# Kernel tuning notes

Hardware: AMD Instinct MI355X
Metric: run time of the kernel (lower is better)

Reference implementation:

```python
import jax, jax.numpy as jnp
import numpy as np

B, CIN, COUT, H, W = 16, 96, 96, 96, 96
K = 3   # hidden_kernels (conv), odd -> same padding
A = 3   # attn_kernels, odd -> stride-1 unfold preserves H*W positions


def _conv(x, w, p):
    # NCHW conv with symmetric padding p, stride 1, no bias
    return jax.lax.conv_general_dilated(
        x, w, window_strides=(1, 1), padding=[(p, p), (p, p)],
        dimension_numbers=("NCHW", "OIHW", "NCHW"))


def _unfold_nonoverlap(y, a):
    # torch nn.Unfold(a, stride=a): [B,C,H,W] -> [B, C*a*a, L], channel-major (c,kh,kw)
    b, c, h, w = y.shape
    hb, wb = h // a, w // a
    y = y.reshape(b, c, hb, a, wb, a).transpose(0, 1, 3, 5, 2, 4)
    return y.reshape(b, c * a * a, hb * wb)


def _unfold_stride1(y, a):
    # torch nn.Unfold(a, padding=a//2): [B,C,H,W] -> [B, C*a*a, H*W]
    b, c, h, w = y.shape
    p = a // 2
    yp = jnp.pad(y, ((0, 0), (0, 0), (p, p), (p, p)))
    # small fixed a*a loop (9 shifts), channel-major (c,kh,kw) ordering
    patches = jnp.stack([yp[:, :, i:i + h, j:j + w]
                         for i in range(a) for j in range(a)], axis=2)
    return patches.reshape(b, c * a * a, h * w)


def setup_inputs() -> dict:
    key = jax.random.key(0)
    kx, k1, k2, k3 = jax.random.split(key, 4)
    x = jax.random.normal(kx, (B, CIN, H, W), dtype=jnp.float32)
    W1 = jax.random.normal(k1, (COUT, CIN, K, K), dtype=jnp.float32) * 0.05
    W2 = jax.random.normal(k2, (COUT, CIN, K, K), dtype=jnp.float32) * 0.05
    W3 = jax.random.normal(k3, (COUT, CIN, K, K), dtype=jnp.float32) * 0.05
    return {"x": x, "W1": W1, "W2": W2, "W3": W3}


def reference(x, W1, W2, W3):
    a, c, p = A, COUT, K // 2
    b = x.shape[0]
    y1 = _unfold_nonoverlap(_conv(x, W1, p), a)   # [B, C*a^2, L]
    y2 = _unfold_nonoverlap(_conv(x, W2, p), a)   # [B, C*a^2, L]
    L = y1.shape[-1]
    y1 = y1.reshape(b, c, a * a, L).transpose(0, 2, 1, 3)  # [B, a^2, C, L]
    y2 = y2.reshape(b, c, a * a, L).transpose(0, 2, 3, 1)  # [B, a^2, L, C]
    attn = jnp.einsum("bkcl,bkld->bkcd", y1, y2)           # [B, a^2, C, C]
    # torch: transpose(1,3).flatten(2) -> [B, C, C*a^2], then scale + softmax(dim=2)
    attn = attn.transpose(0, 3, 2, 1).reshape(b, c, c * a * a)
    attn = jax.nn.softmax(attn / np.float32(np.sqrt(c * a * a)), axis=2)
    v = _unfold_stride1(_conv(x, W3, p), a)        # [B, C*a^2, H*W]
    out = jnp.einsum("bcm,bml->bcl", attn, v)      # [B, C, H*W]
    return out.reshape(b, c, H, W)
```

## Files before the change

### kernel.cpp

```cpp
#include <hip/hip_runtime.h>
#include <math.h>
#include <stdint.h>

constexpr int BB  = 16;
constexpr int CH  = 96;
constexpr int HH  = 96;
constexpr int WW  = 96;
constexpr int HWI = HH * WW;
constexpr int CHW = CH * HWI;
constexpr int IMG = BB * CHW;
constexpr int ATT = BB * CH * CH * 9;
constexpr int WPK = 27 * 6 * 64 * 8;

typedef short short8 __attribute__((ext_vector_type(8)));
typedef float floatx4 __attribute__((ext_vector_type(4)));

__device__ __forceinline__ ushort f2bf(float f) {
  union { float f; unsigned u; } v; v.f = f;
  unsigned r = (v.u + 0x7fffu + ((v.u >> 16) & 1u)) >> 16;
  return (ushort)r;
}
__device__ __forceinline__ float bf2f(ushort h) {
  union { float f; unsigned u; } v; v.u = ((unsigned)h) << 16;
  return v.f;
}

__device__ __forceinline__ void gl_lds_b128(const void* g, void* s) {
  auto gp = (const __attribute__((address_space(1))) void*)(uintptr_t)g;
  auto sp = (__attribute__((address_space(3))) void*)(uintptr_t)s;
  __builtin_amdgcn_global_load_lds(gp, sp, 16, 0, 0);
}

__global__ __launch_bounds__(256) void prepack(
    const float* __restrict__ src, ushort* __restrict__ dst)
{
  const int g = blockIdx.y;
  const int p = blockIdx.x * 256 + threadIdx.x;
  const float* s = src + (size_t)g * WPK;
  ushort* d = dst + (size_t)g * WPK;
  const int j    = p & 7;
  const int lane = (p >> 3) & 63;
  const int rest = p >> 9;
  const int mt = rest % 6;
  const int kc = rest / 6;
  const int m  = mt * 16 + (lane & 15);
  const int k  = kc * 32 + (lane >> 4) * 8 + j;
  const int ci = k % 96;
  const int o  = k / 96;
  d[p] = f2bf(s[m * 864 + ci * 9 + o]);
}

__global__ __launch_bounds__(256, 2) void conv_mfma(
    const float* __restrict__ X, const ushort* __restrict__ Wpk,
    float* __restrict__ Y, int wbstride)
{
  const int b    = blockIdx.y;
  const int tile = blockIdx.x;
  const int ty0  = (tile / 6) * 12;
  const int tx0  = (tile % 6) * 16;
  const int tid  = threadIdx.x;
  const int lane = tid & 63;
  const int w    = tid >> 6;
  const int nc   = lane & 15;
  const int q    = lane >> 4;

  __shared__ __attribute__((aligned(16))) ushort Xs[252 * 104];
  __shared__ __attribute__((aligned(16))) ushort Wl[2][3072];

  const ushort* wp = Wpk + (size_t)b * wbstride;

  {
    gl_lds_b128(wp + w * 512 + lane * 8,
                (ushort*)Wl[0] + __builtin_amdgcn_readfirstlane(w * 512));
    if (w < 2)
      gl_lds_b128(wp + (w + 4) * 512 + lane * 8,
                  (ushort*)Wl[0] + __builtin_amdgcn_readfirstlane((w + 4) * 512));
  }

  if (tid < 252) {
    const int ly = tid / 18, lx = tid % 18;
    const int gy = ty0 - 1 + ly, gx = tx0 - 1 + lx;
    const bool inb = ((unsigned)gy < 96u) & ((unsigned)gx < 96u);
    const float* src = X + (size_t)b * CHW + gy * WW + gx;
    ushort* dst = &Xs[tid * 104];
#pragma unroll 4
    for (int cg = 0; cg < 24; ++cg) {
      float f0 = 0.f, f1 = 0.f, f2 = 0.f, f3 = 0.f;
      if (inb) {
        const float* s = src + (size_t)(cg * 4) * HWI;
        f0 = s[0]; f1 = s[HWI]; f2 = s[2 * HWI]; f3 = s[3 * HWI];
      }
      ushort4 u;
      u.x = f2bf(f0); u.y = f2bf(f1); u.z = f2bf(f2); u.w = f2bf(f3);
      *(ushort4*)(dst + cg * 4) = u;
    }
  }
  __syncthreads();

  floatx4 acc[6][3];
#pragma unroll
  for (int mt = 0; mt < 6; ++mt)
#pragma unroll
    for (int t = 0; t < 3; ++t)
#pragma unroll
      for (int r = 0; r < 4; ++r) acc[mt][t][r] = 0.f;

  for (int ch = 0; ch < 27; ++ch) {
    if (ch < 26) {
      const ushort* src = wp + (size_t)(ch + 1) * 3072;
      ushort* dstb = (ushort*)Wl[(ch + 1) & 1];
      gl_lds_b128(src + w * 512 + lane * 8,
                  dstb + __builtin_amdgcn_readfirstlane(w * 512));
      if (w < 2)
        gl_lds_b128(src + (w + 4) * 512 + lane * 8,
                    dstb + __builtin_amdgcn_readfirstlane((w + 4) * 512));
    }

    const ushort* wb = Wl[ch & 1];
    const int o  = ch / 3;
    const int cc = ch - o * 3;
    const int dy = o / 3, dx = o - dy * 3;
    const int pc = nc + dx;
    const int cib = cc * 32 + q * 8;

    short8 bfr[3];
#pragma unroll
    for (int t = 0; t < 3; ++t) {
      const int pix = (3 * w + t + dy) * 18 + pc;
      bfr[t] = *(const short8*)(&Xs[pix * 104 + cib]);
    }

#pragma unroll
    for (int mt = 0; mt < 6; ++mt) {
      const short8 af = *(const short8*)(wb + mt * 512 + lane * 8);
#pragma unroll
      for (int t = 0; t < 3; ++t)
        acc[mt][t] = __builtin_amdgcn_mfma_f32_16x16x32_bf16(
            af, bfr[t], acc[mt][t], 0, 0, 0);
    }
    __syncthreads();
  }

  float* yb = Y + (size_t)b * CHW;
#pragma unroll
  for (int mt = 0; mt < 6; ++mt)
#pragma unroll
    for (int t = 0; t < 3; ++t) {
      const int yy = ty0 + 3 * w + t;
      const int xx = tx0 + nc;
#pragma unroll
      for (int r = 0; r < 4; ++r) {
        const int co = mt * 16 + q * 4 + r;
        yb[(size_t)co * HWI + yy * WW + xx] = acc[mt][t][r];
      }
    }
}

__global__ __launch_bounds__(256, 2) void conv_dual_mfma(
    const float* __restrict__ X,
    const ushort* __restrict__ WpkA, const ushort* __restrict__ WpkB,
    float* __restrict__ YA, float* __restrict__ YB)
{
  const int b    = blockIdx.y;
  const int tile = blockIdx.x;
  const int ty0  = (tile / 6) * 12;
  const int tx0  = (tile % 6) * 16;
  const int tid  = threadIdx.x;
  const int lane = tid & 63;
  const int w    = tid >> 6;
  const int nc   = lane & 15;
  const int q    = lane >> 4;

  __shared__ __attribute__((aligned(16))) ushort Xs[252 * 104];
  __shared__ __attribute__((aligned(16))) ushort Wl[2][6144];

  {
#pragma unroll
    for (int i = 0; i < 3; ++i) {
      const int p  = w + 4 * i;
      const int cv = p / 6;
      const int pt = p - cv * 6;
      const ushort* src = (cv ? WpkB : WpkA) + pt * 512 + lane * 8;
      gl_lds_b128(src, (ushort*)Wl[0] +
                  __builtin_amdgcn_readfirstlane(cv * 3072 + pt * 512));
    }
  }

  if (tid < 252) {
    const int ly = tid / 18, lx = tid % 18;
    const int gy = ty0 - 1 + ly, gx = tx0 - 1 + lx;
    const bool inb = ((unsigned)gy < 96u) & ((unsigned)gx < 96u);
    const float* src = X + (size_t)b * CHW + gy * WW + gx;
    ushort* dst = &Xs[tid * 104];
#pragma unroll 4
    for (int cg = 0; cg < 24; ++cg) {
      float f0 = 0.f, f1 = 0.f, f2 = 0.f, f3 = 0.f;
      if (inb) {
        const float* s = src + (size_t)(cg * 4) * HWI;
        f0 = s[0]; f1 = s[HWI]; f2 = s[2 * HWI]; f3 = s[3 * HWI];
      }
      ushort4 u;
      u.x = f2bf(f0); u.y = f2bf(f1); u.z = f2bf(f2); u.w = f2bf(f3);
      *(ushort4*)(dst + cg * 4) = u;
    }
  }
  __syncthreads();

  floatx4 accA[6][3], accB[6][3];
#pragma unroll
  for (int mt = 0; mt < 6; ++mt)
#pragma unroll
    for (int t = 0; t < 3; ++t)
#pragma unroll
      for (int r = 0; r < 4; ++r) { accA[mt][t][r] = 0.f; accB[mt][t][r] = 0.f; }

  for (int ch = 0; ch < 27; ++ch) {
    if (ch < 26) {
      const size_t coff = (size_t)(ch + 1) * 3072;
      ushort* dstb = (ushort*)Wl[(ch + 1) & 1];
#pragma unroll
      for (int i = 0; i < 3; ++i) {
        const int p  = w + 4 * i;
        const int cv = p / 6;
        const int pt = p - cv * 6;
        const ushort* src = (cv ? WpkB : WpkA) + coff + pt * 512 + lane * 8;
        gl_lds_b128(src, dstb +
                    __builtin_amdgcn_readfirstlane(cv * 3072 + pt * 512));
      }
    }

    const ushort* wb = Wl[ch & 1];
    const int o  = ch / 3;
    const int cc = ch - o * 3;
    const int dy = o / 3, dx = o - dy * 3;
    const int pc = nc + dx;
    const int cib = cc * 32 + q * 8;

    short8 bfr[3];
#pragma unroll
    for (int t = 0; t < 3; ++t) {
      const int pix = (3 * w + t + dy) * 18 + pc;
      bfr[t] = *(const short8*)(&Xs[pix * 104 + cib]);
    }

#pragma unroll
    for (int mt = 0; mt < 6; ++mt) {
      const short8 afA = *(const short8*)(wb + mt * 512 + lane * 8);
#pragma unroll
      for (int t = 0; t < 3; ++t)
        accA[mt][t] = __builtin_amdgcn_mfma_f32_16x16x32_bf16(
            afA, bfr[t], accA[mt][t], 0, 0, 0);
      const short8 afB = *(const short8*)(wb + 3072 + mt * 512 + lane * 8);
#pragma unroll
      for (int t = 0; t < 3; ++t)
        accB[mt][t] = __builtin_amdgcn_mfma_f32_16x16x32_bf16(
            afB, bfr[t], accB[mt][t], 0, 0, 0);
    }
    __syncthreads();
  }

  float* yA = YA + (size_t)b * CHW;
  float* yB = YB + (size_t)b * CHW;
#pragma unroll
  for (int mt = 0; mt < 6; ++mt)
#pragma unroll
    for (int t = 0; t < 3; ++t) {
      const int yy = ty0 + 3 * w + t;
      const int xx = tx0 + nc;
#pragma unroll
      for (int r = 0; r < 4; ++r) {
        const int co = mt * 16 + q * 4 + r;
        yA[(size_t)co * HWI + yy * WW + xx] = accA[mt][t][r];
        yB[(size_t)co * HWI + yy * WW + xx] = accB[mt][t][r];
      }
    }
}

__global__ __launch_bounds__(1024) void attn_mfma(
    const float* __restrict__ Y1, const float* __restrict__ Y2,
    float* __restrict__ attnT)
{
  const int b  = blockIdx.x / 9;
  const int k  = blockIdx.x % 9;
  const int kh = k / 3, kw = k % 3;
  const int tid  = threadIdx.x;
  const int lane = tid & 63;
  const int wv   = tid >> 6;

  __shared__ ushort Ah[96 * 72], Al[96 * 72], Bh[96 * 72], Bl[96 * 72];

  const float* y1b = Y1 + (size_t)b * CHW;
  const float* y2b = Y2 + (size_t)b * CHW;

  const int mg = wv / 3;
  const int ng = wv % 3;
  const int cn = lane & 15;
  const int q  = lane >> 4;

  floatx4 acc[2][2];
#pragma unroll
  for (int i = 0; i < 2; ++i)
#pragma unroll
    for (int j = 0; j < 2; ++j)
#pragma unroll
      for (int r = 0; r < 4; ++r) acc[i][j][r] = 0.f;

  const int sj = tid & 31;
  const int sg = tid >> 5;
  const int scol = 3 * sj + kw;

  for (int s = 0; s < 16; ++s) {
    __syncthreads();
#pragma unroll
    for (int c8 = 0; c8 < 3; ++c8) {
      const int c = c8 * 32 + sg;
      const int cbase = c * 72;
#pragma unroll
      for (int ii = 0; ii < 2; ++ii) {
        const int row = 3 * (s * 2 + ii) + kh;
        const int p   = ii * 32 + sj;
        const size_t goff = (size_t)c * HWI + row * WW + scol;
        const float v1 = y1b[goff];
        const float v2 = y2b[goff];
        const ushort h1 = f2bf(v1);
        const ushort h2 = f2bf(v2);
        Ah[cbase + p] = h1;
        Al[cbase + p] = f2bf(v1 - bf2f(h1));
        Bh[cbase + p] = h2;
        Bl[cbase + p] = f2bf(v2 - bf2f(h2));
      }
    }
    __syncthreads();

    if (wv < 9) {
#pragma unroll
      for (int kc = 0; kc < 2; ++kc) {
        short8 ah[2], al[2], bh[2], bl[2];
#pragma unroll
        for (int t = 0; t < 2; ++t) {
          const int offA = ((mg * 2 + t) * 16 + cn) * 72 + kc * 32 + q * 8;
          ah[t] = *(const short8*)(&Ah[offA]);
          al[t] = *(const short8*)(&Al[offA]);
          const int offB = ((ng * 2 + t) * 16 + cn) * 72 + kc * 32 + q * 8;
          bh[t] = *(const short8*)(&Bh[offB]);
          bl[t] = *(const short8*)(&Bl[offB]);
        }
#pragma unroll
        for (int i = 0; i < 2; ++i)
#pragma unroll
          for (int j = 0; j < 2; ++j) {
            acc[i][j] = __builtin_amdgcn_mfma_f32_16x16x32_bf16(
                ah[i], bh[j], acc[i][j], 0, 0, 0);
            acc[i][j] = __builtin_amdgcn_mfma_f32_16x16x32_bf16(
                ah[i], bl[j], acc[i][j], 0, 0, 0);
            acc[i][j] = __builtin_amdgcn_mfma_f32_16x16x32_bf16(
                al[i], bh[j], acc[i][j], 0, 0, 0);
          }
      }
    }
  }

  if (wv < 9) {
#pragma unroll
    for (int i = 0; i < 2; ++i)
#pragma unroll
      for (int j = 0; j < 2; ++j)
#pragma unroll
        for (int r = 0; r < 4; ++r) {
          const int c = (mg * 2 + i) * 16 + q * 4 + r;
          const int d = (ng * 2 + j) * 16 + cn;
          attnT[((size_t)(b * CH + d) * CH + c) * 9 + k] = acc[i][j][r];
        }
  }
}

__global__ __launch_bounds__(256) void softmax_k(
    const float* __restrict__ attnT, float* __restrict__ attnW)
{
  const int bd = blockIdx.x;
  const float* src = attnT + (size_t)bd * 864;
  float* dst = attnW + (size_t)bd * 864;
  const float rs = 0.0340216824f;
  const int tid = threadIdx.x;

  float v0 = src[tid];
  float v1 = src[tid + 256];
  float v2 = src[tid + 512];
  float v3 = (tid < 96) ? src[tid + 768] : -3.0e38f;

  float mx = fmaxf(fmaxf(v0, v1), fmaxf(v2, v3));

  __shared__ float red[256];
  red[tid] = mx;
  __syncthreads();
#pragma unroll
  for (int s = 128; s > 0; s >>= 1) {
    if (tid < s) red[tid] = fmaxf(red[tid], red[tid + s]);
    __syncthreads();
  }
  mx = red[0];
  __syncthreads();

  const float e0 = expf((v0 - mx) * rs);
  const float e1 = expf((v1 - mx) * rs);
  const float e2 = expf((v2 - mx) * rs);
  const float e3 = (tid < 96) ? expf((v3 - mx) * rs) : 0.f;

  red[tid] = e0 + e1 + e2 + e3;
  __syncthreads();
#pragma unroll
  for (int s = 128; s > 0; s >>= 1) {
    if (tid < s) red[tid] += red[tid + s];
    __syncthreads();
  }
  const float inv = 1.f / red[0];

  dst[tid]       = e0 * inv;
  dst[tid + 256] = e1 * inv;
  dst[tid + 512] = e2 * inv;
  if (tid < 96) dst[tid + 768] = e3 * inv;
}

extern "C" void kernel_launch(void* const* d_in, const int* in_sizes, int n_in,
                              void* d_out, int out_size, void* d_ws, size_t ws_size,
                              hipStream_t stream)
{
  const float* x  = (const float*)d_in[0];
  const float* W1 = (const float*)d_in[1];
  const float* W2 = (const float*)d_in[2];
  const float* W3 = (const float*)d_in[3];

  float* ws    = (float*)d_ws;
  float* Y1    = ws;
  float* Y2    = ws + (size_t)IMG;
  float* attnT = ws + 2 * (size_t)IMG;
  float* attnW = attnT + ATT;
  ushort* pk   = (ushort*)(ws + 2 * (size_t)IMG + 2 * (size_t)ATT);
  ushort* pkW1 = pk;
  ushort* pkW2 = pk + WPK;
  ushort* pkW3 = pk + 2 * (size_t)WPK;
  ushort* pkAW = pk + 3 * (size_t)WPK;
  float* Y3    = Y1;

  const dim3 cgrid(48, BB);

  prepack  <<<dim3(324, 1),  256, 0, stream>>>(W1, pkW1);
  prepack  <<<dim3(324, 1),  256, 0, stream>>>(W2, pkW2);
  prepack  <<<dim3(324, 1),  256, 0, stream>>>(W3, pkW3);

  conv_dual_mfma<<<cgrid, 256, 0, stream>>>(x, pkW1, pkW2, Y1, Y2);

  attn_mfma<<<BB * 9, 1024, 0, stream>>>(Y1, Y2, attnT);
  softmax_k<<<BB * CH, 256, 0, stream>>>(attnT, attnW);

  prepack  <<<dim3(324, BB), 256, 0, stream>>>(attnW, pkAW);

  conv_mfma<<<cgrid, 256, 0, stream>>>(x, pkW3, Y3, 0);
  conv_mfma<<<cgrid, 256, 0, stream>>>(Y3, pkAW, (float*)d_out, WPK);
}
```

Measured before the change: 370.6 us.

## Split attention reduction over spatial chunks, pre-split hi/lo bf16, store Y3 as bf16

The attention Gram kernel now splits the spatial reduction into four chunks, launching four times as many smaller 256-thread blocks. Each block writes a partial result, and the softmax kernel sums the four partials before normalizing. The dual conv now writes hi/lo bf16 pairs packed in a uint, so the attention kernel no longer does that conversion. The intermediate V conv output is stored as bf16 through a templated conv kernel, which halves its memory traffic. Partial buffers reuse the output and workspace as scratch, which adds extra partial-sum reads and relies on careful aliasing of attnW as both a partial buffer and the softmax output.

```diff
diff --git a/kernel.cpp b/kernel.cpp
--- a/kernel.cpp
+++ b/kernel.cpp
@@ -23,6 +23,11 @@
 __device__ __forceinline__ float bf2f(ushort h) {
   union { float f; unsigned u; } v; v.u = ((unsigned)h) << 16;
   return v.f;
+}
+__device__ __forceinline__ uint packhl(float v) {
+  const ushort h = f2bf(v);
+  const ushort l = f2bf(v - bf2f(h));
+  return (uint)h | ((uint)l << 16);
 }
 
 __device__ __forceinline__ void gl_lds_b128(const void* g, void* s) {
@@ -50,9 +55,10 @@
   d[p] = f2bf(s[m * 864 + ci * 9 + o]);
 }
 
-__global__ __launch_bounds__(256, 2) void conv_mfma(
-    const float* __restrict__ X, const ushort* __restrict__ Wpk,
-    float* __restrict__ Y, int wbstride)
+template<bool INBF, bool OUTBF>
+__global__ __launch_bounds__(256, 2) void conv_mfma_t(
+    const void* __restrict__ Xv, const ushort* __restrict__ Wpk,
+    void* __restrict__ Yv, int wbstride)
 {
   const int b    = blockIdx.y;
   const int tile = blockIdx.x;
@@ -75,6 +81,132 @@
     if (w < 2)
       gl_lds_b128(wp + (w + 4) * 512 + lane * 8,
                   (ushort*)Wl[0] + __builtin_amdgcn_readfirstlane((w + 4) * 512));
+  }
+
+  if (tid < 252) {
+    const int ly = tid / 18, lx = tid % 18;
+    const int gy = ty0 - 1 + ly, gx = tx0 - 1 + lx;
+    const bool inb = ((unsigned)gy < 96u) & ((unsigned)gx < 96u);
+    ushort* dst = &Xs[tid * 104];
+    if constexpr (INBF) {
+      const ushort* src = (const ushort*)Xv + (size_t)b * CHW + gy * WW + gx;
+#pragma unroll 4
+      for (int cg = 0; cg < 24; ++cg) {
+        ushort u0 = 0, u1 = 0, u2 = 0, u3 = 0;
+        if (inb) {
+          const ushort* s = src + (size_t)(cg * 4) * HWI;
+          u0 = s[0]; u1 = s[HWI]; u2 = s[2 * HWI]; u3 = s[3 * HWI];
+        }
+        ushort4 u; u.x = u0; u.y = u1; u.z = u2; u.w = u3;
+        *(ushort4*)(dst + cg * 4) = u;
+      }
+    } else {
+      const float* src = (const float*)Xv + (size_t)b * CHW + gy * WW + gx;
+#pragma unroll 4
+      for (int cg = 0; cg < 24; ++cg) {
+        float f0 = 0.f, f1 = 0.f, f2 = 0.f, f3 = 0.f;
+        if (inb) {
+          const float* s = src + (size_t)(cg * 4) * HWI;
+          f0 = s[0]; f1 = s[HWI]; f2 = s[2 * HWI]; f3 = s[3 * HWI];
+        }
+        ushort4 u;
+        u.x = f2bf(f0); u.y = f2bf(f1); u.z = f2bf(f2); u.w = f2bf(f3);
+        *(ushort4*)(dst + cg * 4) = u;
+      }
+    }
+  }
+  __syncthreads();
+
+  floatx4 acc[6][3];
+#pragma unroll
+  for (int mt = 0; mt < 6; ++mt)
+#pragma unroll
+    for (int t = 0; t < 3; ++t)
+#pragma unroll
+      for (int r = 0; r < 4; ++r) acc[mt][t][r] = 0.f;
+
+  for (int ch = 0; ch < 27; ++ch) {
+    if (ch < 26) {
+      const ushort* src = wp + (size_t)(ch + 1) * 3072;
+      ushort* dstb = (ushort*)Wl[(ch + 1) & 1];
+      gl_lds_b128(src + w * 512 + lane * 8,
+                  dstb + __builtin_amdgcn_readfirstlane(w * 512));
+      if (w < 2)
+        gl_lds_b128(src + (w + 4) * 512 + lane * 8,
+                    dstb + __builtin_amdgcn_readfirstlane((w + 4) * 512));
+    }
+
+    const ushort* wb = Wl[ch & 1];
+    const int o  = ch / 3;
+    const int cc = ch - o * 3;
+    const int dy = o / 3, dx = o - dy * 3;
+    const int pc = nc + dx;
+    const int cib = cc * 32 + q * 8;
+
+    short8 bfr[3];
+#pragma unroll
+    for (int t = 0; t < 3; ++t) {
+      const int pix = (3 * w + t + dy) * 18 + pc;
+      bfr[t] = *(const short8*)(&Xs[pix * 104 + cib]);
+    }
+
+#pragma unroll
+    for (int mt = 0; mt < 6; ++mt) {
+      const short8 af = *(const short8*)(wb + mt * 512 + lane * 8);
+#pragma unroll
+      for (int t = 0; t < 3; ++t)
+        acc[mt][t] = __builtin_amdgcn_mfma_f32_16x16x32_bf16(
+            af, bfr[t], acc[mt][t], 0, 0, 0);
+    }
+    __syncthreads();
+  }
+
+#pragma unroll
+  for (int mt = 0; mt < 6; ++mt)
+#pragma unroll
+    for (int t = 0; t < 3; ++t) {
+      const int yy = ty0 + 3 * w + t;
+      const int xx = tx0 + nc;
+#pragma unroll
+      for (int r = 0; r < 4; ++r) {
+        const int co = mt * 16 + q * 4 + r;
+        const size_t off = (size_t)co * HWI + yy * WW + xx;
+        if constexpr (OUTBF)
+          ((ushort*)Yv + (size_t)b * CHW)[off] = f2bf(acc[mt][t][r]);
+        else
+          ((float*)Yv + (size_t)b * CHW)[off] = acc[mt][t][r];
+      }
+    }
+}
+
+__global__ __launch_bounds__(256, 2) void conv_dual_mfma(
+    const float* __restrict__ X,
+    const ushort* __restrict__ WpkA, const ushort* __restrict__ WpkB,
+    uint* __restrict__ YA, uint* __restrict__ YB)
+{
+  const int b    = blockIdx.y;
+  const int tile = blockIdx.x;
+  const int ty0  = (tile / 6) * 12;
+  const int tx0  = (tile % 6) * 16;
+  const int tid  = threadIdx.x;
+  const int lane = tid & 63;
+  const int w    = tid >> 6;
+  const int nc   = lane & 15;
+  const int q    = lane >> 4;
+
+  __shared__ __attribute__((aligned(16))) ushort Xs[252 * 104];
+  __shared__ __attribute__((aligned(16))) ushort Wl[2][6144];
+
+  {
+#pragma unroll
+    for (int i = 0; i < 3; ++i) {
+      const int p  = w + 4 * i;
+      const int cv = p / 6;
+      const int pt = p - cv * 6;
+      const ushort* src = (cv ? WpkB : WpkA) + pt * 512 + lane * 8;
+      gl_lds_b128(src, (ushort*)Wl[0] +
+                  __builtin_amdgcn_readfirstlane(cv * 3072 + pt * 512));
+    }
   }
 
   if (tid < 252) {
@@ -97,115 +229,6 @@
   }
   __syncthreads();
 
-  floatx4 acc[6][3];
-#pragma unroll
-  for (int mt = 0; mt < 6; ++mt)
-#pragma unroll
-    for (int t = 0; t < 3; ++t)
-#pragma unroll
-      for (int r = 0; r < 4; ++r) acc[mt][t][r] = 0.f;
-
-  for (int ch = 0; ch < 27; ++ch) {
-    if (ch < 26) {
-      const ushort* src = wp + (size_t)(ch + 1) * 3072;
-      ushort* dstb = (ushort*)Wl[(ch + 1) & 1];
-      gl_lds_b128(src + w * 512 + lane * 8,
-                  dstb + __builtin_amdgcn_readfirstlane(w * 512));
-      if (w < 2)
-        gl_lds_b128(src + (w + 4) * 512 + lane * 8,
-                    dstb + __builtin_amdgcn_readfirstlane((w + 4) * 512));
-    }
-
-    const ushort* wb = Wl[ch & 1];
-    const int o  = ch / 3;
-    const int cc = ch - o * 3;
-    const int dy = o / 3, dx = o - dy * 3;
-    const int pc = nc + dx;
-    const int cib = cc * 32 + q * 8;
-
-    short8 bfr[3];
-#pragma unroll
-    for (int t = 0; t < 3; ++t) {
-      const int pix = (3 * w + t + dy) * 18 + pc;
-      bfr[t] = *(const short8*)(&Xs[pix * 104 + cib]);
-    }
-
-#pragma unroll
-    for (int mt = 0; mt < 6; ++mt) {
-      const short8 af = *(const short8*)(wb + mt * 512 + lane * 8);
-#pragma unroll
-      for (int t = 0; t < 3; ++t)
-        acc[mt][t] = __builtin_amdgcn_mfma_f32_16x16x32_bf16(
-            af, bfr[t], acc[mt][t], 0, 0, 0);
-    }
-    __syncthreads();
-  }
-
-  float* yb = Y + (size_t)b * CHW;
-#pragma unroll
-  for (int mt = 0; mt < 6; ++mt)
-#pragma unroll
-    for (int t = 0; t < 3; ++t) {
-      const int yy = ty0 + 3 * w + t;
-      const int xx = tx0 + nc;
-#pragma unroll
-      for (int r = 0; r < 4; ++r) {
-        const int co = mt * 16 + q * 4 + r;
-        yb[(size_t)co * HWI + yy * WW + xx] = acc[mt][t][r];
-      }
-    }
-}
-
-__global__ __launch_bounds__(256, 2) void conv_dual_mfma(
-    const float* __restrict__ X,
-    const ushort* __restrict__ WpkA, const ushort* __restrict__ WpkB,
-    float* __restrict__ YA, float* __restrict__ YB)
-{
-  const int b    = blockIdx.y;
-  const int tile = blockIdx.x;
-  const int ty0  = (tile / 6) * 12;
-  const int tx0  = (tile % 6) * 16;
-  const int tid  = threadIdx.x;
-  const int lane = tid & 63;
-  const int w    = tid >> 6;
-  const int nc   = lane & 15;
-  const int q    = lane >> 4;
-
-  __shared__ __attribute__((aligned(16))) ushort Xs[252 * 104];
-  __shared__ __attribute__((aligned(16))) ushort Wl[2][6144];
-
-  {
-#pragma unroll
-    for (int i = 0; i < 3; ++i) {
-      const int p  = w + 4 * i;
-      const int cv = p / 6;
-      const int pt = p - cv * 6;
-      const ushort* src = (cv ? WpkB : WpkA) + pt * 512 + lane * 8;
-      gl_lds_b128(src, (ushort*)Wl[0] +
-                  __builtin_amdgcn_readfirstlane(cv * 3072 + pt * 512));
-    }
-  }
-
-  if (tid < 252) {
-    const int ly = tid / 18, lx = tid % 18;
-    const int gy = ty0 - 1 + ly, gx = tx0 - 1 + lx;
-    const bool inb = ((unsigned)gy < 96u) & ((unsigned)gx < 96u);
-    const float* src = X + (size_t)b * CHW + gy * WW + gx;
-    ushort* dst = &Xs[tid * 104];
-#pragma unroll 4
-    for (int cg = 0; cg < 24; ++cg) {
-      float f0 = 0.f, f1 = 0.f, f2 = 0.f, f3 = 0.f;
-      if (inb) {
-        const float* s = src + (size_t)(cg * 4) * HWI;
-        f0 = s[0]; f1 = s[HWI]; f2 = s[2 * HWI]; f3 = s[3 * HWI];
-      }
-      ushort4 u;
-      u.x = f2bf(f0); u.y = f2bf(f1); u.z = f2bf(f2); u.w = f2bf(f3);
-      *(ushort4*)(dst + cg * 4) = u;
-    }
-  }
-  __syncthreads();
-
   floatx4 accA[6][3], accB[6][3];
 #pragma unroll
   for (int mt = 0; mt < 6; ++mt)
@@ -259,8 +282,8 @@
     __syncthreads();
   }
 
-  float* yA = YA + (size_t)b * CHW;
-  float* yB = YB + (size_t)b * CHW;
+  uint* yA = YA + (size_t)b * CHW;
+  uint* yB = YB + (size_t)b * CHW;
 #pragma unroll
   for (int mt = 0; mt < 6; ++mt)
 #pragma unroll
@@ -270,18 +293,22 @@
 #pragma unroll
       for (int r = 0; r < 4; ++r) {
         const int co = mt * 16 + q * 4 + r;
-        yA[(size_t)co * HWI + yy * WW + xx] = accA[mt][t][r];
-        yB[(size_t)co * HWI + yy * WW + xx] = accB[mt][t][r];
-      }
-    }
-}
-
-__global__ __launch_bounds__(1024) void attn_mfma(
-    const float* __restrict__ Y1, const float* __restrict__ Y2,
-    float* __restrict__ attnT)
-{
-  const int b  = blockIdx.x / 9;
-  const int k  = blockIdx.x % 9;
+        yA[(size_t)co * HWI + yy * WW + xx] = packhl(accA[mt][t][r]);
+        yB[(size_t)co * HWI + yy * WW + xx] = packhl(accB[mt][t][r]);
+      }
+    }
+}
+
+__global__ __launch_bounds__(256) void attn_mfma(
+    const uint* __restrict__ Y1, const uint* __restrict__ Y2,
+    float* __restrict__ P0, float* __restrict__ P1,
+    float* __restrict__ P2, float* __restrict__ P3)
+{
+  const int bi = blockIdx.x;
+  const int b  = bi / 36;
+  const int r9 = bi % 36;
+  const int k  = r9 >> 2;
+  const int qd = r9 & 3;
   const int kh = k / 3, kw = k % 3;
   const int tid  = threadIdx.x;
   const int lane = tid & 63;
@@ -289,19 +316,19 @@
 
   __shared__ ushort Ah[96 * 72], Al[96 * 72], Bh[96 * 72], Bl[96 * 72];
 
-  const float* y1b = Y1 + (size_t)b * CHW;
-  const float* y2b = Y2 + (size_t)b * CHW;
-
-  const int mg = wv / 3;
-  const int ng = wv % 3;
+  const uint* y1b = Y1 + (size_t)b * CHW;
+  const uint* y2b = Y2 + (size_t)b * CHW;
+
+  const int mg2 = wv >> 1;
+  const int ng2 = wv & 1;
   const int cn = lane & 15;
   const int q  = lane >> 4;
 
-  floatx4 acc[2][2];
-#pragma unroll
-  for (int i = 0; i < 2; ++i)
-#pragma unroll
-    for (int j = 0; j < 2; ++j)
+  floatx4 acc[3][3];
+#pragma unroll
+  for (int i = 0; i < 3; ++i)
+#pragma unroll
+    for (int j = 0; j < 3; ++j)
 #pragma unroll
       for (int r = 0; r < 4; ++r) acc[i][j][r] = 0.f;
 
@@ -309,84 +336,85 @@
   const int sg = tid >> 5;
   const int scol = 3 * sj + kw;
 
-  for (int s = 0; s < 16; ++s) {
-    __syncthreads();
-#pragma unroll
-    for (int c8 = 0; c8 < 3; ++c8) {
-      const int c = c8 * 32 + sg;
+  for (int ss = 0; ss < 4; ++ss) {
+    const int s = qd * 4 + ss;
+    __syncthreads();
+#pragma unroll
+    for (int cg = 0; cg < 12; ++cg) {
+      const int c = cg * 8 + sg;
       const int cbase = c * 72;
 #pragma unroll
       for (int ii = 0; ii < 2; ++ii) {
         const int row = 3 * (s * 2 + ii) + kh;
         const int p   = ii * 32 + sj;
         const size_t goff = (size_t)c * HWI + row * WW + scol;
-        const float v1 = y1b[goff];
-        const float v2 = y2b[goff];
-        const ushort h1 = f2bf(v1);
-        const ushort h2 = f2bf(v2);
-        Ah[cbase + p] = h1;
-        Al[cbase + p] = f2bf(v1 - bf2f(h1));
-        Bh[cbase + p] = h2;
-        Bl[cbase + p] = f2bf(v2 - bf2f(h2));
-      }
-    }
-    __syncthreads();
-
-    if (wv < 9) {
-#pragma unroll
-      for (int kc = 0; kc < 2; ++kc) {
-        short8 ah[2], al[2], bh[2], bl[2];
-#pragma unroll
-        for (int t = 0; t < 2; ++t) {
-          const int offA = ((mg * 2 + t) * 16 + cn) * 72 + kc * 32 + q * 8;
-          ah[t] = *(const short8*)(&Ah[offA]);
-          al[t] = *(const short8*)(&Al[offA]);
-          const int offB = ((ng * 2 + t) * 16 + cn) * 72 + kc * 32 + q * 8;
-          bh[t] = *(const short8*)(&Bh[offB]);
-          bl[t] = *(const short8*)(&Bl[offB]);
+        const uint u1 = y1b[goff];
+        const uint u2 = y2b[goff];
+        Ah[cbase + p] = (ushort)(u1 & 0xffffu);
+        Al[cbase + p] = (ushort)(u1 >> 16);
+        Bh[cbase + p] = (ushort)(u2 & 0xffffu);
+        Bl[cbase + p] = (ushort)(u2 >> 16);
+      }
+    }
+    __syncthreads();
+
+#pragma unroll
+    for (int kc = 0; kc < 2; ++kc) {
+      short8 ah[3], al[3], bh[3], bl[3];
+#pragma unroll
+      for (int t = 0; t < 3; ++t) {
+        const int offA = (mg2 * 48 + t * 16 + cn) * 72 + kc * 32 + q * 8;
+        ah[t] = *(const short8*)(&Ah[offA]);
+        al[t] = *(const short8*)(&Al[offA]);
+        const int offB = (ng2 * 48 + t * 16 + cn) * 72 + kc * 32 + q * 8;
+        bh[t] = *(const short8*)(&Bh[offB]);
+        bl[t] = *(const short8*)(&Bl[offB]);
+      }
+#pragma unroll
+      for (int i = 0; i < 3; ++i)
+#pragma unroll
+        for (int j = 0; j < 3; ++j) {
+          acc[i][j] = __builtin_amdgcn_mfma_f32_16x16x32_bf16(
+              ah[i], bh[j], acc[i][j], 0, 0, 0);
+          acc[i][j] = __builtin_amdgcn_mfma_f32_16x16x32_bf16(
+              ah[i], bl[j], acc[i][j], 0, 0, 0);
+          acc[i][j] = __builtin_amdgcn_mfma_f32_16x16x32_bf16(
+              al[i], bh[j], acc[i][j], 0, 0, 0);
         }
-#pragma unroll
-        for (int i = 0; i < 2; ++i)
-#pragma unroll
-          for (int j = 0; j < 2; ++j) {
-            acc[i][j] = __builtin_amdgcn_mfma_f32_16x16x32_bf16(
-                ah[i], bh[j], acc[i][j], 0, 0, 0);
-            acc[i][j] = __builtin_amdgcn_mfma_f32_16x16x32_bf16(
-                ah[i], bl[j], acc[i][j], 0, 0, 0);
-            acc[i][j] = __builtin_amdgcn_mfma_f32_16x16x32_bf16(
-                al[i], bh[j], acc[i][j], 0, 0, 0);
-          }
-      }
-    }
-  }
-
-  if (wv < 9) {
-#pragma unroll
-    for (int i = 0; i < 2; ++i)
-#pragma unroll
-      for (int j = 0; j < 2; ++j)
-#pragma unroll
-        for (int r = 0; r < 4; ++r) {
-          const int c = (mg * 2 + i) * 16 + q * 4 + r;
-          const int d = (ng * 2 + j) * 16 + cn;
-          attnT[((size_t)(b * CH + d) * CH + c) * 9 + k] = acc[i][j][r];
-        }
-  }
+    }
+  }
+
+  float* P = (qd == 0) ? P0 : (qd == 1) ? P1 : (qd == 2) ? P2 : P3;
+#pragma unroll
+  for (int i = 0; i < 3; ++i)
+#pragma unroll
+    for (int j = 0; j < 3; ++j)
+#pragma unroll
+      for (int r = 0; r < 4; ++r) {
+        const int c = mg2 * 48 + i * 16 + q * 4 + r;
+        const int d = ng2 * 48 + j * 16 + cn;
+        P[((size_t)(b * CH + d) * CH + c) * 9 + k] = acc[i][j][r];
+      }
 }
 
 __global__ __launch_bounds__(256) void softmax_k(
-    const float* __restrict__ attnT, float* __restrict__ attnW)
+    const float* __restrict__ P0, const float* __restrict__ P1,
+    const float* __restrict__ P2, const float* __restrict__ P3,
+    float* __restrict__ attnW)
 {
   const int bd = blockIdx.x;
-  const float* src = attnT + (size_t)bd * 864;
-  float* dst = attnW + (size_t)bd * 864;
+  const size_t base = (size_t)bd * 864;
+  float* dst = attnW + base;
   const float rs = 0.0340216824f;
   const int tid = threadIdx.x;
 
-  float v0 = src[tid];
-  float v1 = src[tid + 256];
-  float v2 = src[tid + 512];
-  float v3 = (tid < 96) ? src[tid + 768] : -3.0e38f;
+  const size_t i0 = base + tid;
+  float v0 = P0[i0] + P1[i0] + P2[i0] + P3[i0];
+  float v1 = P0[i0 + 256] + P1[i0 + 256] + P2[i0 + 256] + P3[i0 + 256];
+  float v2 = P0[i0 + 512] + P1[i0 + 512] + P2[i0 + 512] + P3[i0 + 512];
+  float v3 = (tid < 96)
+      ? (P0[i0 + 768] + P1[i0 + 768] + P2[i0 + 768] + P3[i0 + 768])
+      : -3.0e38f;
 
   float mx = fmaxf(fmaxf(v0, v1), fmaxf(v2, v3));
 
@@ -431,8 +459,8 @@
   const float* W3 = (const float*)d_in[3];
 
   float* ws    = (float*)d_ws;
-  float* Y1    = ws;
-  float* Y2    = ws + (size_t)IMG;
+  uint*  Y1    = (uint*)ws;
+  uint*  Y2    = (uint*)(ws + (size_t)IMG);
   float* attnT = ws + 2 * (size_t)IMG;
   float* attnW = attnT + ATT;
   ushort* pk   = (ushort*)(ws + 2 * (size_t)IMG + 2 * (size_t)ATT);
@@ -440,7 +468,9 @@
   ushort* pkW2 = pk + WPK;
   ushort* pkW3 = pk + 2 * (size_t)WPK;
   ushort* pkAW = pk + 3 * (size_t)WPK;
-  float* Y3    = Y1;
+  float* Pd2   = (float*)d_out;
+  float* Pd3   = Pd2 + ATT;
+  ushort* Y3bf = (ushort*)ws;
 
   const dim3 cgrid(48, BB);
 
@@ -450,11 +480,11 @@
 
   conv_dual_mfma<<<cgrid, 256, 0, stream>>>(x, pkW1, pkW2, Y1, Y2);
 
-  attn_mfma<<<BB * 9, 1024, 0, stream>>>(Y1, Y2, attnT);
-  softmax_k<<<BB * CH, 256, 0, stream>>>(attnT, attnW);
+  attn_mfma<<<BB * 9 * 4, 256, 0, stream>>>(Y1, Y2, attnT, attnW, Pd2, Pd3);
+  softmax_k<<<BB * CH, 256, 0, stream>>>(attnT, attnW, Pd2, Pd3, attnW);
 
   prepack  <<<dim3(324, BB), 256, 0, stream>>>(attnW, pkAW);
 
-  conv_mfma<<<cgrid, 256, 0, stream>>>(x, pkW3, Y3, 0);
-  conv_mfma<<<cgrid, 256, 0, stream>>>(Y3, pkAW, (float*)d_out, WPK);
-}
+  conv_mfma_t<false, true><<<cgrid, 256, 0, stream>>>(x, pkW3, Y3bf, 0);
+  conv_mfma_t<true, false><<<cgrid, 256, 0, stream>>>(Y3bf, pkAW, d_out, WPK);
+}
```

New measurement: 399.6 us. 7.8% more time.
